# Optimization experiments

Measured on AMD Instinct MI355X. Metric: run time of the kernel, lower is better.

## Reference

```python
import jax, jax.numpy as jnp
import numpy as np

DIM = 16
BOND = 4
RANK = 512
N = 50000
E = 400000
F_IN = 16
EDGE_VARIABLE = 2


def setup_inputs() -> dict:
    key = jax.random.key(0)
    ks = iter(jax.random.split(key, 48))
    g = lambda shape, s=0.1: jax.random.normal(next(ks), shape, jnp.float32) * s
    inp = {
        "x": jax.random.normal(next(ks), (N, F_IN), jnp.float32),
        "node_type": jax.random.randint(next(ks), (N,), 0, 3),
        "edge_index": jax.random.randint(next(ks), (2, E), 0, N),
        "edge_attr": jax.random.uniform(next(ks), (E, BOND), dtype=jnp.float32),
        # lin0
        "W_lin0": g((F_IN, DIM)), "b_lin0": jnp.zeros((DIM,), jnp.float32),
        # NNConv: root weight + edge-conditioned weight MLP (4 -> 32 -> dim*dim)
        "W_root": g((DIM, DIM)), "b_conv": jnp.zeros((DIM,), jnp.float32),
        "W_e1": g((BOND, 32)), "b_e1": jnp.zeros((32,), jnp.float32),
        "W_e2": g((32, DIM * DIM)), "b_e2": jnp.zeros((DIM * DIM,), jnp.float32),
        # GRU (torch gate order r,z,n), weights stored torch-style [3*dim, dim]
        "W_ih": g((3 * DIM, DIM)), "b_ih": jnp.zeros((3 * DIM,), jnp.float32),
        "W_hh": g((3 * DIM, DIM)), "b_hh": jnp.zeros((3 * DIM,), jnp.float32),
        # projections
        "W_lin1": g((DIM, BOND)), "b_lin1": jnp.zeros((BOND,), jnp.float32),
        "W_up": g((BOND, DIM)), "b_up": jnp.zeros((DIM,), jnp.float32),
        "W_down": g((DIM, BOND)), "b_down": jnp.zeros((BOND,), jnp.float32),
        # FGNet low-rank factor modules (rank 512)
        "U_B": g((DIM, RANK)), "V_B": g((RANK, DIM)),
        "U_C": g((DIM, RANK)), "V_C": g((RANK, DIM)),
        "U_A": g((BOND, RANK)), "V_A": g((RANK, BOND)),
        # fusion weights
        "w_node": g((1, DIM)), "W_lin": g((DIM, DIM)), "b_lin": jnp.zeros((DIM,), jnp.float32),
        "w_edge": g((1, BOND)), "W_line": g((BOND, BOND)), "b_line": jnp.zeros((BOND,), jnp.float32),
    }
    return inp


def _forward(x, edge_attr, W_lin0, b_lin0, W_root, b_conv, W_e1, b_e1, W_e2, b_e2,
             W_ih, b_ih, W_hh, b_hh, W_lin1, b_lin1, W_up, b_up, W_down, b_down,
             U_B, V_B, U_C, V_C, U_A, V_A, w_node, W_lin, b_lin, w_edge, W_line, b_line,
             node_type, edge_index):
    src, dst = edge_index[0], edge_index[1]

    def nnconv(out):
        # per-edge weight matrices from edge features (edge-conditioned conv)
        he = jax.nn.relu(edge_attr @ W_e1 + b_e1)
        We = (he @ W_e2 + b_e2).reshape(E, DIM, DIM)          # [E, dim, dim]
        m = jnp.einsum('ed,edk->ek', out[src], We)             # gather-multiply
        agg = jax.ops.segment_sum(m, dst, num_segments=N)      # scatter-add
        deg = jax.ops.segment_sum(jnp.ones((E,), out.dtype), dst, num_segments=N)
        agg = agg / jnp.clip(deg, 1.0)[:, None]                # mean aggregation
        return out @ W_root + b_conv + agg

    def gru(inp, h):
        gi = inp @ W_ih.T + b_ih
        gh = h @ W_hh.T + b_hh
        i_r, i_z, i_n = jnp.split(gi, 3, axis=-1)
        h_r, h_z, h_n = jnp.split(gh, 3, axis=-1)
        r = jax.nn.sigmoid(i_r + h_r)
        z = jax.nn.sigmoid(i_z + h_z)
        n = jnp.tanh(i_n + r * h_n)
        return (1.0 - z) * n + z * h

    out = jax.nn.relu(x @ W_lin0 + b_lin0)                     # [N, dim]
    h = out
    for _ in range(3):
        m = jax.nn.relu(nnconv(out))
        h = gru(m, h)
        out = h

    out_edges = jax.nn.relu(out @ W_lin1 + b_lin1)             # [N, bond]

    # one outer message-passing round (k in range(1))
    ev_mask = (node_type == EDGE_VARIABLE)[:, None]
    out_edges_up = out_edges @ W_up + b_up                     # [N, dim]
    out_combine = jnp.where(ev_mask, out_edges_up, out)        # masked replace

    # factor-B message (low-rank FGNet) -> node-dim message + down-projected edge msg
    msg_B = jax.nn.relu((out_combine @ U_B) @ V_B)             # [N, dim]
    msg_to_edge_B = msg_B @ W_down + b_down                    # [N, bond]

    # factor-C message (low-rank FGNet)
    msg_C = jax.nn.relu((out_combine @ U_C) @ V_C)             # [N, dim]

    # factor-A / valence message on edge-type beliefs
    msg_to_edge_A = jax.nn.relu((out_edges @ U_A) @ V_A)       # [N, bond]

    all_msg = msg_B + msg_C                                    # sum over stacked msgs
    combine_edge_msg = msg_to_edge_A * msg_to_edge_B

    out = out + jax.nn.relu((w_node * all_msg) @ W_lin + b_lin)
    out_edges = out_edges + jax.nn.relu((w_edge * combine_edge_msg) @ W_line + b_line)

    return jax.nn.log_softmax(out_edges, axis=-1)              # [N, bond]


def reference(x, node_type, edge_index, edge_attr, W_lin0, b_lin0, W_root, b_conv,
              W_e1, b_e1, W_e2, b_e2, W_ih, b_ih, W_hh, b_hh, W_lin1, b_lin1,
              W_up, b_up, W_down, b_down, U_B, V_B, U_C, V_C, U_A, V_A,
              w_node, W_lin, b_lin, w_edge, W_line, b_line):
    return _forward(x, edge_attr, W_lin0, b_lin0, W_root, b_conv, W_e1, b_e1, W_e2, b_e2,
                    W_ih, b_ih, W_hh, b_hh, W_lin1, b_lin1, W_up, b_up, W_down, b_down,
                    U_B, V_B, U_C, V_C, U_A, V_A, w_node, W_lin, b_lin, w_edge, W_line, b_line,
                    node_type, edge_index)
```

## Files before the change

### kernel.cpp

```cpp
#include <hip/hip_runtime.h>
#include <hip/hip_bf16.h>
#include <math.h>

#define N_NODES 50000
#define N_EDGES 400000
#define DIM 16
#define BOND 4
#define NCHUNK 25000
#define EDGE_GRID 784
#define E_BLOCKS 1563
#define PRE_BASE (E_BLOCKS - 68)
#define SCAN_TILE 1024
#define SCAN_BLOCKS 49

typedef __attribute__((ext_vector_type(8))) short short8;
typedef __attribute__((ext_vector_type(4))) float f32x4;

__device__ __forceinline__ float bf16_to_f32(unsigned short v) {
  return __uint_as_float(((unsigned int)v) << 16);
}

__global__ __launch_bounds__(256) void setup_kernel(
    const float* __restrict__ x, const float* __restrict__ W_lin0,
    const float* __restrict__ b_lin0, const float* __restrict__ ea,
    const float* __restrict__ We1, const float* __restrict__ be1,
    const int* __restrict__ ei, const float* __restrict__ U_B,
    const float* __restrict__ V_B, const float* __restrict__ U_A,
    const float* __restrict__ V_A, float* __restrict__ out,
    unsigned int* __restrict__ he_buf, int* __restrict__ degI,
    int* __restrict__ rank, float* __restrict__ M_B, float* __restrict__ M_A) {
  __shared__ float sW0[256];
  __shared__ float sb0[16];
  __shared__ float sW1[128];
  __shared__ float sb1[32];
  int t = threadIdx.x;
  sW0[t] = W_lin0[t];
  if (t < 16) sb0[t] = b_lin0[t];
  if (t < 128) sW1[t] = We1[t];
  if (t < 32) sb1[t] = be1[t];
  __syncthreads();

  int gid = blockIdx.x * 256 + t;

  if (gid < N_NODES) {
    float xr[16];
#pragma unroll
    for (int d = 0; d < 16; ++d) xr[d] = x[gid * 16 + d];
#pragma unroll
    for (int k = 0; k < 16; ++k) {
      float acc = sb0[k];
#pragma unroll
      for (int d = 0; d < 16; ++d) acc += xr[d] * sW0[d * 16 + k];
      out[gid * 16 + k] = fmaxf(acc, 0.f);
    }
  }

  if (gid < N_EDGES) {
    float4 v = ((const float4*)ea)[gid];
    float h[32];
#pragma unroll
    for (int k = 0; k < 32; ++k) {
      float a = sb1[k] + v.x * sW1[k] + v.y * sW1[32 + k] + v.z * sW1[64 + k] +
                v.w * sW1[96 + k];
      h[k] = fmaxf(a, 0.f);
    }
    unsigned int u[16];
#pragma unroll
    for (int p = 0; p < 2; ++p)
#pragma unroll
      for (int tt = 0; tt < 8; ++tt) {
        float2 pr;
        pr.x = h[4 * tt + p];
        pr.y = h[4 * tt + 2 + p];
        __hip_bfloat162 b = __float22bfloat162_rn(pr);
        u[p * 8 + tt] = *(unsigned int*)&b;
      }
    uint4* dst = (uint4*)(he_buf + (size_t)gid * 16);
#pragma unroll
    for (int qq = 0; qq < 4; ++qq)
      dst[qq] =
          make_uint4(u[4 * qq], u[4 * qq + 1], u[4 * qq + 2], u[4 * qq + 3]);
    rank[gid] = atomicAdd(&degI[ei[N_EDGES + gid]], 1);
  }

  if (blockIdx.x >= PRE_BASE) {
    int w = (blockIdx.x - PRE_BASE) * 4 + (t >> 6);
    int lane = t & 63;
    float partial = 0.f;
    if (w < 256) {
      int i = w >> 4, j = w & 15;
#pragma unroll
      for (int r8 = 0; r8 < 8; ++r8) {
        int r = lane + 64 * r8;
        partial += U_B[i * 512 + r] * V_B[r * 16 + j];
      }
    } else if (w < 272) {
      int a = (w - 256) >> 2, b = (w - 256) & 3;
#pragma unroll
      for (int r8 = 0; r8 < 8; ++r8) {
        int r = lane + 64 * r8;
        partial += U_A[a * 512 + r] * V_A[r * 4 + b];
      }
    }
#pragma unroll
    for (int off = 32; off > 0; off >>= 1)
      partial += __shfl_down(partial, off);
    if (lane == 0) {
      if (w < 256) M_B[w] = partial;
      else if (w < 272) M_A[w - 256] = partial;
    }
  }
}

__global__ __launch_bounds__(256) void scan_kernel(
    const int* __restrict__ degI, int* ticket, int* st,
    int* __restrict__ row_off) {
  __shared__ int sdata[256];
  __shared__ int s_tile;
  __shared__ int s_base;
  int t = threadIdx.x;
  if (t == 0) s_tile = atomicAdd(ticket, 1);
  __syncthreads();
  int tile = s_tile;
  int n0 = tile * SCAN_TILE + t * 4;

  int d0 = (n0 + 0 < N_NODES) ? degI[n0 + 0] : 0;
  int d1 = (n0 + 1 < N_NODES) ? degI[n0 + 1] : 0;
  int d2 = (n0 + 2 < N_NODES) ? degI[n0 + 2] : 0;
  int d3 = (n0 + 3 < N_NODES) ? degI[n0 + 3] : 0;
  int tsum = d0 + d1 + d2 + d3;
  sdata[t] = tsum;
  __syncthreads();
  for (int off = 1; off < 256; off <<= 1) {
    int v = (t >= off) ? sdata[t - off] : 0;
    __syncthreads();
    sdata[t] += v;
    __syncthreads();
  }
  int excl = sdata[t] - tsum;
  int agg = sdata[255];

  if (t == 0) {
    if (tile == 0) {
      atomicExch(&st[0], (agg << 2) | 2);
      s_base = 0;
    } else {
      atomicExch(&st[tile], (agg << 2) | 1);
      int run = 0, idx = tile - 1;
      while (true) {
        int w = atomicAdd(&st[idx], 0);
        int stt = w & 3;
        if (stt == 2) { run += (w >> 2); break; }
        if (stt == 1) { run += (w >> 2); --idx; }
      }
      atomicExch(&st[tile], ((run + agg) << 2) | 2);
      s_base = run;
    }
  }
  __syncthreads();

  int pre = s_base + excl;
  if (n0 + 0 < N_NODES) row_off[n0 + 0] = pre;
  pre += d0;
  if (n0 + 1 < N_NODES) row_off[n0 + 1] = pre;
  pre += d1;
  if (n0 + 2 < N_NODES) row_off[n0 + 2] = pre;
  pre += d2;
  if (n0 + 3 < N_NODES) row_off[n0 + 3] = pre;
  if (tile == SCAN_BLOCKS - 1 && t == 0) row_off[N_NODES] = N_EDGES;
}

__global__ __launch_bounds__(256) void slot_kernel(
    const int* __restrict__ ei, const int* __restrict__ row_off,
    const int* __restrict__ rank, int* __restrict__ slot) {
  int e = blockIdx.x * 256 + threadIdx.x;
  if (e < N_EDGES) slot[e] = row_off[ei[N_EDGES + e]] + rank[e];
}

__global__ __launch_bounds__(256) void edge_msg_mfma_kernel(
    const int* __restrict__ ei, const unsigned int* __restrict__ he_buf,
    const float* __restrict__ We2, const float* __restrict__ be2,
    const float* __restrict__ out, const int* __restrict__ slot,
    unsigned short* __restrict__ m_bufh) {
  const int lane = threadIdx.x & 63;
  const int q = lane >> 4, n = lane & 15;
  const int p = q >> 1, dbase = (q & 1) * 8;

  short8 bfrag[17];
#pragma unroll
  for (int s = 0; s < 16; ++s) {
    int h = 2 * s + p;
    union { short8 v; __hip_bfloat162 b2[4]; } bf;
#pragma unroll
    for (int jj = 0; jj < 4; ++jj) {
      float2 w;
      w.x = We2[h * 256 + (dbase + 2 * jj) * 16 + n];
      w.y = We2[h * 256 + (dbase + 2 * jj + 1) * 16 + n];
      bf.b2[jj] = __float22bfloat162_rn(w);
    }
    bfrag[s] = bf.v;
  }
  {
    union { short8 v; __hip_bfloat162 b2[4]; } bf;
#pragma unroll
    for (int jj = 0; jj < 4; ++jj) {
      float2 w;
      if (q < 2) {
        w.x = be2[(dbase + 2 * jj) * 16 + n];
        w.y = be2[(dbase + 2 * jj + 1) * 16 + n];
      } else {
        w.x = 0.f; w.y = 0.f;
      }
      bf.b2[jj] = __float22bfloat162_rn(w);
    }
    bfrag[16] = bf.v;
  }

  int wave = blockIdx.x * 4 + (threadIdx.x >> 6);
  const int nw = EDGE_GRID * 4;
  for (int c = wave; c < NCHUNK; c += nw) {
    int e = c * 16 + n;
    int src = ei[e];
    const uint4* hp = (const uint4*)(he_buf + (size_t)e * 16 + p * 8);
    uint4 h0 = hp[0], h1 = hp[1];
    unsigned int heu[8] = {h0.x, h0.y, h0.z, h0.w, h1.x, h1.y, h1.z, h1.w};
    const float4* op = (const float4*)(out + src * 16 + dbase);
    float4 o0 = op[0], o1 = op[1];
    float o[8] = {o0.x, o0.y, o0.z, o0.w, o1.x, o1.y, o1.z, o1.w};

    f32x4 acc = {0.f, 0.f, 0.f, 0.f};
#pragma unroll
    for (int s = 0; s < 16; ++s) {
      unsigned int hw = heu[s >> 1];
      float he_s = __uint_as_float((s & 1) ? (hw & 0xffff0000u) : (hw << 16));
      union { short8 v; __hip_bfloat162 b2[4]; } af;
#pragma unroll
      for (int jj = 0; jj < 4; ++jj) {
        float2 pr;
        pr.x = he_s * o[2 * jj];
        pr.y = he_s * o[2 * jj + 1];
        af.b2[jj] = __float22bfloat162_rn(pr);
      }
      acc = __builtin_amdgcn_mfma_f32_16x16x32_bf16(af.v, bfrag[s], acc, 0, 0, 0);
    }
    {
      union { short8 v; __hip_bfloat162 b2[4]; } af;
#pragma unroll
      for (int jj = 0; jj < 4; ++jj) {
        float2 pr;
        if (q < 2) { pr.x = o[2 * jj]; pr.y = o[2 * jj + 1]; }
        else { pr.x = 0.f; pr.y = 0.f; }
        af.b2[jj] = __float22bfloat162_rn(pr);
      }
      acc = __builtin_amdgcn_mfma_f32_16x16x32_bf16(af.v, bfrag[16], acc, 0, 0, 0);
    }

    int4 sl4 = *(const int4*)(slot + c * 16 + q * 4);
    __hip_bfloat16 b0 = __float2bfloat16(acc[0]);
    __hip_bfloat16 b1 = __float2bfloat16(acc[1]);
    __hip_bfloat16 b2 = __float2bfloat16(acc[2]);
    __hip_bfloat16 b3 = __float2bfloat16(acc[3]);
    m_bufh[(size_t)sl4.x * 16 + n] = *(unsigned short*)&b0;
    m_bufh[(size_t)sl4.y * 16 + n] = *(unsigned short*)&b1;
    m_bufh[(size_t)sl4.z * 16 + n] = *(unsigned short*)&b2;
    m_bufh[(size_t)sl4.w * 16 + n] = *(unsigned short*)&b3;
  }
}

__global__ __launch_bounds__(256) void gather_gru_kernel(
    const int* __restrict__ row_off, const unsigned short* __restrict__ m_bufh,
    const float* __restrict__ Wroot, const float* __restrict__ bconv,
    const float* __restrict__ Wih, const float* __restrict__ bih,
    const float* __restrict__ Whh, const float* __restrict__ bhh,
    float* __restrict__ out, int do_final, const int* __restrict__ node_type,
    const float* __restrict__ Wlin1, const float* __restrict__ blin1,
    const float* __restrict__ Wup, const float* __restrict__ bup,
    const float* __restrict__ Wdown, const float* __restrict__ bdown,
    const float* __restrict__ M_B, const float* __restrict__ M_A,
    const float* __restrict__ wedge, const float* __restrict__ Wline,
    const float* __restrict__ bline, float* __restrict__ res) {
  __shared__ float sWr[256];
  __shared__ float sWihT[768];
  __shared__ float sWhhT[768];
  __shared__ float sb[112];
  int t = threadIdx.x;
  int kk = t >> 4, dd = t & 15;
  sWr[t] = Wroot[t];
#pragma unroll
  for (int g = 0; g < 3; ++g) {
    sWihT[g * 256 + dd * 16 + kk] = Wih[g * 256 + t];
    sWhhT[g * 256 + dd * 16 + kk] = Whh[g * 256 + t];
  }
  if (t < 16) sb[t] = bconv[t];
  else if (t < 64) sb[t] = bih[t - 16];
  else if (t < 112) sb[t] = bhh[t - 64];
  __syncthreads();

  int n = blockIdx.x * 16 + (t >> 4);
  int k = t & 15;
  int s0 = row_off[n], s1 = row_off[n + 1];

  float aggk = 0.f;
  for (int j = s0; j < s1; ++j) aggk += bf16_to_f32(m_bufh[(size_t)j * 16 + k]);
  float sc = 1.f / fmaxf((float)(s1 - s0), 1.f);

  float hk = out[n * 16 + k];

  float mk = sb[k] + aggk * sc;
#pragma unroll
  for (int d = 0; d < 16; ++d) mk += __shfl(hk, d, 16) * sWr[d * 16 + k];
  mk = fmaxf(mk, 0.f);

  float gir = sb[16 + k], giz = sb[32 + k], gin = sb[48 + k];
  float ghr = sb[64 + k], ghz = sb[80 + k], ghn = sb[96 + k];
#pragma unroll
  for (int d = 0; d < 16; ++d) {
    float md = __shfl(mk, d, 16);
    float hd = __shfl(hk, d, 16);
    gir += md * sWihT[d * 16 + k];
    giz += md * sWihT[256 + d * 16 + k];
    gin += md * sWihT[512 + d * 16 + k];
    ghr += hd * sWhhT[d * 16 + k];
    ghz += hd * sWhhT[256 + d * 16 + k];
    ghn += hd * sWhhT[512 + d * 16 + k];
  }
  float r = 1.f / (1.f + __expf(-(gir + ghr)));
  float z = 1.f / (1.f + __expf(-(giz + ghz)));
  float xn = gin + r * ghn;
  float ng = 1.f - 2.f / (__expf(2.f * xn) + 1.f);
  float hnew = (1.f - z) * ng + z * hk;

  if (!do_final) {
    out[n * 16 + k] = hnew;
    return;
  }

  float p0 = hnew * Wlin1[k * 4 + 0];
  float p1 = hnew * Wlin1[k * 4 + 1];
  float p2 = hnew * Wlin1[k * 4 + 2];
  float p3 = hnew * Wlin1[k * 4 + 3];
#pragma unroll
  for (int msk = 1; msk < 16; msk <<= 1) {
    p0 += __shfl_xor(p0, msk, 16);
    p1 += __shfl_xor(p1, msk, 16);
    p2 += __shfl_xor(p2, msk, 16);
    p3 += __shfl_xor(p3, msk, 16);
  }
  float oe0 = fmaxf(p0 + blin1[0], 0.f);
  float oe1 = fmaxf(p1 + blin1[1], 0.f);
  float oe2 = fmaxf(p2 + blin1[2], 0.f);
  float oe3 = fmaxf(p3 + blin1[3], 0.f);

  bool ev = (node_type[n] == 2);
  float ock = ev ? (bup[k] + oe0 * Wup[k] + oe1 * Wup[16 + k] +
                    oe2 * Wup[32 + k] + oe3 * Wup[48 + k])
                 : hnew;

  float msgBk = 0.f;
#pragma unroll
  for (int d = 0; d < 16; ++d) msgBk += __shfl(ock, d, 16) * M_B[d * 16 + k];
  msgBk = fmaxf(msgBk, 0.f);

  float q0 = msgBk * Wdown[k * 4 + 0];
  float q1 = msgBk * Wdown[k * 4 + 1];
  float q2 = msgBk * Wdown[k * 4 + 2];
  float q3 = msgBk * Wdown[k * 4 + 3];
#pragma unroll
  for (int msk = 1; msk < 16; msk <<= 1) {
    q0 += __shfl_xor(q0, msk, 16);
    q1 += __shfl_xor(q1, msk, 16);
    q2 += __shfl_xor(q2, msk, 16);
    q3 += __shfl_xor(q3, msk, 16);
  }
  float mtb0 = q0 + bdown[0], mtb1 = q1 + bdown[1];
  float mtb2 = q2 + bdown[2], mtb3 = q3 + bdown[3];

  float mta0 = fmaxf(oe0 * M_A[0] + oe1 * M_A[4] + oe2 * M_A[8] + oe3 * M_A[12], 0.f);
  float mta1 = fmaxf(oe0 * M_A[1] + oe1 * M_A[5] + oe2 * M_A[9] + oe3 * M_A[13], 0.f);
  float mta2 = fmaxf(oe0 * M_A[2] + oe1 * M_A[6] + oe2 * M_A[10] + oe3 * M_A[14], 0.f);
  float mta3 = fmaxf(oe0 * M_A[3] + oe1 * M_A[7] + oe2 * M_A[11] + oe3 * M_A[15], 0.f);

  float c0 = wedge[0] * (mta0 * mtb0);
  float c1 = wedge[1] * (mta1 * mtb1);
  float c2 = wedge[2] * (mta2 * mtb2);
  float c3 = wedge[3] * (mta3 * mtb3);

  float f0 = oe0 + fmaxf(bline[0] + c0 * Wline[0] + c1 * Wline[4] +
                         c2 * Wline[8] + c3 * Wline[12], 0.f);
  float f1 = oe1 + fmaxf(bline[1] + c0 * Wline[1] + c1 * Wline[5] +
                         c2 * Wline[9] + c3 * Wline[13], 0.f);
  float f2 = oe2 + fmaxf(bline[2] + c0 * Wline[2] + c1 * Wline[6] +
                         c2 * Wline[10] + c3 * Wline[14], 0.f);
  float f3 = oe3 + fmaxf(bline[3] + c0 * Wline[3] + c1 * Wline[7] +
                         c2 * Wline[11] + c3 * Wline[15], 0.f);

  float mx = fmaxf(fmaxf(f0, f1), fmaxf(f2, f3));
  float se = __expf(f0 - mx) + __expf(f1 - mx) + __expf(f2 - mx) +
             __expf(f3 - mx);
  float lse = mx + __logf(se);
  if (k < 4) {
    float v = (k == 0) ? f0 : (k == 1) ? f1 : (k == 2) ? f2 : f3;
    res[n * 4 + k] = v - lse;
  }
}

extern "C" void kernel_launch(void* const* d_in, const int* in_sizes, int n_in,
                              void* d_out, int out_size, void* d_ws,
                              size_t ws_size, hipStream_t stream) {
  const float* x       = (const float*)d_in[0];
  const int* node_type = (const int*)d_in[1];
  const int* ei        = (const int*)d_in[2];
  const float* ea      = (const float*)d_in[3];
  const float* W_lin0  = (const float*)d_in[4];
  const float* b_lin0  = (const float*)d_in[5];
  const float* W_root  = (const float*)d_in[6];
  const float* b_conv  = (const float*)d_in[7];
  const float* W_e1    = (const float*)d_in[8];
  const float* b_e1    = (const float*)d_in[9];
  const float* W_e2    = (const float*)d_in[10];
  const float* b_e2    = (const float*)d_in[11];
  const float* W_ih    = (const float*)d_in[12];
  const float* b_ih    = (const float*)d_in[13];
  const float* W_hh    = (const float*)d_in[14];
  const float* b_hh    = (const float*)d_in[15];
  const float* W_lin1  = (const float*)d_in[16];
  const float* b_lin1  = (const float*)d_in[17];
  const float* W_up    = (const float*)d_in[18];
  const float* b_up    = (const float*)d_in[19];
  const float* W_down  = (const float*)d_in[20];
  const float* b_down  = (const float*)d_in[21];
  const float* U_B     = (const float*)d_in[22];
  const float* V_B     = (const float*)d_in[23];
  const float* U_A     = (const float*)d_in[26];
  const float* V_A     = (const float*)d_in[27];
  const float* w_edge  = (const float*)d_in[31];
  const float* W_line  = (const float*)d_in[32];
  const float* b_line  = (const float*)d_in[33];

  float* ws    = (float*)d_ws;
  float* out   = ws;
  unsigned int* he_buf = (unsigned int*)(out + N_NODES * 16);
  unsigned short* m_bufh =
      (unsigned short*)(he_buf + (size_t)N_EDGES * 16);
  float* M_B   = (float*)(m_bufh + (size_t)N_EDGES * 16);
  float* M_A   = M_B + 256;
  int* degI    = (int*)(M_A + 16);
  int* ticket  = degI + N_NODES;
  int* st      = ticket + 1;
  int* row_off = st + 63;
  int* rank    = row_off + N_NODES + 1;
  int* slot    = rank + N_EDGES;

  hipMemsetAsync(degI, 0, (N_NODES + 64) * sizeof(int), stream);

  setup_kernel<<<E_BLOCKS, 256, 0, stream>>>(
      x, W_lin0, b_lin0, ea, W_e1, b_e1, ei, U_B, V_B, U_A, V_A, out, he_buf,
      degI, rank, M_B, M_A);
  scan_kernel<<<SCAN_BLOCKS, 256, 0, stream>>>(degI, ticket, st, row_off);
  slot_kernel<<<E_BLOCKS, 256, 0, stream>>>(ei, row_off, rank, slot);

  for (int it = 0; it < 3; ++it) {
    edge_msg_mfma_kernel<<<EDGE_GRID, 256, 0, stream>>>(ei, he_buf, W_e2, b_e2,
                                                        out, slot, m_bufh);
    gather_gru_kernel<<<N_NODES / 16, 256, 0, stream>>>(
        row_off, m_bufh, W_root, b_conv, W_ih, b_ih, W_hh, b_hh, out,
        (it == 2) ? 1 : 0, node_type, W_lin1, b_lin1, W_up, b_up, W_down,
        b_down, M_B, M_A, w_edge, W_line, b_line, (float*)d_out);
  }
}
```

Baseline: 330.1 us.

## Fuse scan, slot, and three message/GRU iterations into one persistent kernel

```diff
diff --git a/kernel.cpp b/kernel.cpp
--- a/kernel.cpp
+++ b/kernel.cpp
@@ -7,17 +7,43 @@
 #define DIM 16
 #define BOND 4
 #define NCHUNK 25000
-#define EDGE_GRID 784
 #define E_BLOCKS 1563
 #define PRE_BASE (E_BLOCKS - 68)
 #define SCAN_TILE 1024
 #define SCAN_BLOCKS 49
+#define FUSED_BLOCKS 768
+#define NGROUPS 3125
 
 typedef __attribute__((ext_vector_type(8))) short short8;
 typedef __attribute__((ext_vector_type(4))) float f32x4;
 
 __device__ __forceinline__ float bf16_to_f32(unsigned short v) {
   return __uint_as_float(((unsigned int)v) << 16);
+}
+
+__device__ __forceinline__ void grid_sync(int* bar_count, int* bar_gen) {
+  __syncthreads();
+  if (threadIdx.x == 0) {
+    __threadfence();
+    int g = __hip_atomic_load(bar_gen, __ATOMIC_RELAXED, __HIP_MEMORY_SCOPE_AGENT);
+    int old = __hip_atomic_fetch_add(bar_count, 1, __ATOMIC_ACQ_REL,
+                                     __HIP_MEMORY_SCOPE_AGENT);
+    if (old == FUSED_BLOCKS - 1) {
+      __hip_atomic_store(bar_count, 0, __ATOMIC_RELAXED,
+                         __HIP_MEMORY_SCOPE_AGENT);
+      __hip_atomic_fetch_add(bar_gen, 1, __ATOMIC_RELEASE,
+                             __HIP_MEMORY_SCOPE_AGENT);
+    } else {
+      long long t0 = clock64();
+      while (__hip_atomic_load(bar_gen, __ATOMIC_RELAXED,
+                               __HIP_MEMORY_SCOPE_AGENT) == g) {
+        __builtin_amdgcn_s_sleep(2);
+        if (clock64() - t0 > 100000000LL) break;
+      }
+    }
+    __threadfence();
+  }
+  __syncthreads();
 }
 
 __global__ __launch_bounds__(256) void setup_kernel(
@@ -112,77 +138,44 @@
   }
 }
 
-__global__ __launch_bounds__(256) void scan_kernel(
-    const int* __restrict__ degI, int* ticket, int* st,
-    int* __restrict__ row_off) {
-  __shared__ int sdata[256];
-  __shared__ int s_tile;
-  __shared__ int s_base;
-  int t = threadIdx.x;
-  if (t == 0) s_tile = atomicAdd(ticket, 1);
-  __syncthreads();
-  int tile = s_tile;
-  int n0 = tile * SCAN_TILE + t * 4;
-
-  int d0 = (n0 + 0 < N_NODES) ? degI[n0 + 0] : 0;
-  int d1 = (n0 + 1 < N_NODES) ? degI[n0 + 1] : 0;
-  int d2 = (n0 + 2 < N_NODES) ? degI[n0 + 2] : 0;
-  int d3 = (n0 + 3 < N_NODES) ? degI[n0 + 3] : 0;
-  int tsum = d0 + d1 + d2 + d3;
-  sdata[t] = tsum;
-  __syncthreads();
-  for (int off = 1; off < 256; off <<= 1) {
-    int v = (t >= off) ? sdata[t - off] : 0;
-    __syncthreads();
-    sdata[t] += v;
-    __syncthreads();
-  }
-  int excl = sdata[t] - tsum;
-  int agg = sdata[255];
-
-  if (t == 0) {
-    if (tile == 0) {
-      atomicExch(&st[0], (agg << 2) | 2);
-      s_base = 0;
-    } else {
-      atomicExch(&st[tile], (agg << 2) | 1);
-      int run = 0, idx = tile - 1;
-      while (true) {
-        int w = atomicAdd(&st[idx], 0);
-        int stt = w & 3;
-        if (stt == 2) { run += (w >> 2); break; }
-        if (stt == 1) { run += (w >> 2); --idx; }
-      }
-      atomicExch(&st[tile], ((run + agg) << 2) | 2);
-      s_base = run;
-    }
-  }
-  __syncthreads();
-
-  int pre = s_base + excl;
-  if (n0 + 0 < N_NODES) row_off[n0 + 0] = pre;
-  pre += d0;
-  if (n0 + 1 < N_NODES) row_off[n0 + 1] = pre;
-  pre += d1;
-  if (n0 + 2 < N_NODES) row_off[n0 + 2] = pre;
-  pre += d2;
-  if (n0 + 3 < N_NODES) row_off[n0 + 3] = pre;
-  if (tile == SCAN_BLOCKS - 1 && t == 0) row_off[N_NODES] = N_EDGES;
-}
-
-__global__ __launch_bounds__(256) void slot_kernel(
-    const int* __restrict__ ei, const int* __restrict__ row_off,
-    const int* __restrict__ rank, int* __restrict__ slot) {
-  int e = blockIdx.x * 256 + threadIdx.x;
-  if (e < N_EDGES) slot[e] = row_off[ei[N_EDGES + e]] + rank[e];
-}
-
-__global__ __launch_bounds__(256) void edge_msg_mfma_kernel(
+__global__ __launch_bounds__(256, 3) void fused_kernel(
     const int* __restrict__ ei, const unsigned int* __restrict__ he_buf,
     const float* __restrict__ We2, const float* __restrict__ be2,
-    const float* __restrict__ out, const int* __restrict__ slot,
-    unsigned short* __restrict__ m_bufh) {
-  const int lane = threadIdx.x & 63;
+    float* __restrict__ out, unsigned short* __restrict__ m_bufh,
+    const int* __restrict__ degI, int* __restrict__ row_off,
+    const int* __restrict__ rank, int* __restrict__ slot,
+    int* __restrict__ st, int* __restrict__ bar_count,
+    int* __restrict__ bar_gen,
+    const float* __restrict__ Wroot, const float* __restrict__ bconv,
+    const float* __restrict__ Wih, const float* __restrict__ bih,
+    const float* __restrict__ Whh, const float* __restrict__ bhh,
+    const int* __restrict__ node_type, const float* __restrict__ Wlin1,
+    const float* __restrict__ blin1, const float* __restrict__ Wup,
+    const float* __restrict__ bup, const float* __restrict__ Wdown,
+    const float* __restrict__ bdown, const float* __restrict__ M_B,
+    const float* __restrict__ M_A, const float* __restrict__ wedge,
+    const float* __restrict__ Wline, const float* __restrict__ bline,
+    float* __restrict__ res) {
+  __shared__ float sWr[256];
+  __shared__ float sWihT[768];
+  __shared__ float sWhhT[768];
+  __shared__ float sb[112];
+  __shared__ int sdata[256];
+  int t = threadIdx.x;
+  {
+    int kk = t >> 4, dd = t & 15;
+    sWr[t] = Wroot[t];
+#pragma unroll
+    for (int g = 0; g < 3; ++g) {
+      sWihT[g * 256 + dd * 16 + kk] = Wih[g * 256 + t];
+      sWhhT[g * 256 + dd * 16 + kk] = Whh[g * 256 + t];
+    }
+    if (t < 16) sb[t] = bconv[t];
+    else if (t < 64) sb[t] = bih[t - 16];
+    else if (t < 112) sb[t] = bhh[t - 64];
+  }
+
+  const int lane = t & 63;
   const int q = lane >> 4, n = lane & 15;
   const int p = q >> 1, dbase = (q & 1) * 8;
 
@@ -215,192 +208,232 @@
     }
     bfrag[16] = bf.v;
   }
-
-  int wave = blockIdx.x * 4 + (threadIdx.x >> 6);
-  const int nw = EDGE_GRID * 4;
-  for (int c = wave; c < NCHUNK; c += nw) {
-    int e = c * 16 + n;
-    int src = ei[e];
-    const uint4* hp = (const uint4*)(he_buf + (size_t)e * 16 + p * 8);
-    uint4 h0 = hp[0], h1 = hp[1];
-    unsigned int heu[8] = {h0.x, h0.y, h0.z, h0.w, h1.x, h1.y, h1.z, h1.w};
-    const float4* op = (const float4*)(out + src * 16 + dbase);
-    float4 o0 = op[0], o1 = op[1];
-    float o[8] = {o0.x, o0.y, o0.z, o0.w, o1.x, o1.y, o1.z, o1.w};
-
-    f32x4 acc = {0.f, 0.f, 0.f, 0.f};
-#pragma unroll
-    for (int s = 0; s < 16; ++s) {
-      unsigned int hw = heu[s >> 1];
-      float he_s = __uint_as_float((s & 1) ? (hw & 0xffff0000u) : (hw << 16));
-      union { short8 v; __hip_bfloat162 b2[4]; } af;
-#pragma unroll
-      for (int jj = 0; jj < 4; ++jj) {
-        float2 pr;
-        pr.x = he_s * o[2 * jj];
-        pr.y = he_s * o[2 * jj + 1];
-        af.b2[jj] = __float22bfloat162_rn(pr);
-      }
-      acc = __builtin_amdgcn_mfma_f32_16x16x32_bf16(af.v, bfrag[s], acc, 0, 0, 0);
-    }
-    {
-      union { short8 v; __hip_bfloat162 b2[4]; } af;
-#pragma unroll
-      for (int jj = 0; jj < 4; ++jj) {
-        float2 pr;
-        if (q < 2) { pr.x = o[2 * jj]; pr.y = o[2 * jj + 1]; }
-        else { pr.x = 0.f; pr.y = 0.f; }
-        af.b2[jj] = __float22bfloat162_rn(pr);
-      }
-      acc = __builtin_amdgcn_mfma_f32_16x16x32_bf16(af.v, bfrag[16], acc, 0, 0, 0);
-    }
-
-    int4 sl4 = *(const int4*)(slot + c * 16 + q * 4);
-    __hip_bfloat16 b0 = __float2bfloat16(acc[0]);
-    __hip_bfloat16 b1 = __float2bfloat16(acc[1]);
-    __hip_bfloat16 b2 = __float2bfloat16(acc[2]);
-    __hip_bfloat16 b3 = __float2bfloat16(acc[3]);
-    m_bufh[(size_t)sl4.x * 16 + n] = *(unsigned short*)&b0;
-    m_bufh[(size_t)sl4.y * 16 + n] = *(unsigned short*)&b1;
-    m_bufh[(size_t)sl4.z * 16 + n] = *(unsigned short*)&b2;
-    m_bufh[(size_t)sl4.w * 16 + n] = *(unsigned short*)&b3;
-  }
-}
-
-__global__ __launch_bounds__(256) void gather_gru_kernel(
-    const int* __restrict__ row_off, const unsigned short* __restrict__ m_bufh,
-    const float* __restrict__ Wroot, const float* __restrict__ bconv,
-    const float* __restrict__ Wih, const float* __restrict__ bih,
-    const float* __restrict__ Whh, const float* __restrict__ bhh,
-    float* __restrict__ out, int do_final, const int* __restrict__ node_type,
-    const float* __restrict__ Wlin1, const float* __restrict__ blin1,
-    const float* __restrict__ Wup, const float* __restrict__ bup,
-    const float* __restrict__ Wdown, const float* __restrict__ bdown,
-    const float* __restrict__ M_B, const float* __restrict__ M_A,
-    const float* __restrict__ wedge, const float* __restrict__ Wline,
-    const float* __restrict__ bline, float* __restrict__ res) {
-  __shared__ float sWr[256];
-  __shared__ float sWihT[768];
-  __shared__ float sWhhT[768];
-  __shared__ float sb[112];
-  int t = threadIdx.x;
-  int kk = t >> 4, dd = t & 15;
-  sWr[t] = Wroot[t];
-#pragma unroll
-  for (int g = 0; g < 3; ++g) {
-    sWihT[g * 256 + dd * 16 + kk] = Wih[g * 256 + t];
-    sWhhT[g * 256 + dd * 16 + kk] = Whh[g * 256 + t];
-  }
-  if (t < 16) sb[t] = bconv[t];
-  else if (t < 64) sb[t] = bih[t - 16];
-  else if (t < 112) sb[t] = bhh[t - 64];
   __syncthreads();
 
-  int n = blockIdx.x * 16 + (t >> 4);
-  int k = t & 15;
-  int s0 = row_off[n], s1 = row_off[n + 1];
-
-  float aggk = 0.f;
-  for (int j = s0; j < s1; ++j) aggk += bf16_to_f32(m_bufh[(size_t)j * 16 + k]);
-  float sc = 1.f / fmaxf((float)(s1 - s0), 1.f);
-
-  float hk = out[n * 16 + k];
-
-  float mk = sb[k] + aggk * sc;
-#pragma unroll
-  for (int d = 0; d < 16; ++d) mk += __shfl(hk, d, 16) * sWr[d * 16 + k];
-  mk = fmaxf(mk, 0.f);
-
-  float gir = sb[16 + k], giz = sb[32 + k], gin = sb[48 + k];
-  float ghr = sb[64 + k], ghz = sb[80 + k], ghn = sb[96 + k];
-#pragma unroll
-  for (int d = 0; d < 16; ++d) {
-    float md = __shfl(mk, d, 16);
-    float hd = __shfl(hk, d, 16);
-    gir += md * sWihT[d * 16 + k];
-    giz += md * sWihT[256 + d * 16 + k];
-    gin += md * sWihT[512 + d * 16 + k];
-    ghr += hd * sWhhT[d * 16 + k];
-    ghz += hd * sWhhT[256 + d * 16 + k];
-    ghn += hd * sWhhT[512 + d * 16 + k];
-  }
-  float r = 1.f / (1.f + __expf(-(gir + ghr)));
-  float z = 1.f / (1.f + __expf(-(giz + ghz)));
-  float xn = gin + r * ghn;
-  float ng = 1.f - 2.f / (__expf(2.f * xn) + 1.f);
-  float hnew = (1.f - z) * ng + z * hk;
-
-  if (!do_final) {
-    out[n * 16 + k] = hnew;
-    return;
-  }
-
-  float p0 = hnew * Wlin1[k * 4 + 0];
-  float p1 = hnew * Wlin1[k * 4 + 1];
-  float p2 = hnew * Wlin1[k * 4 + 2];
-  float p3 = hnew * Wlin1[k * 4 + 3];
-#pragma unroll
-  for (int msk = 1; msk < 16; msk <<= 1) {
-    p0 += __shfl_xor(p0, msk, 16);
-    p1 += __shfl_xor(p1, msk, 16);
-    p2 += __shfl_xor(p2, msk, 16);
-    p3 += __shfl_xor(p3, msk, 16);
-  }
-  float oe0 = fmaxf(p0 + blin1[0], 0.f);
-  float oe1 = fmaxf(p1 + blin1[1], 0.f);
-  float oe2 = fmaxf(p2 + blin1[2], 0.f);
-  float oe3 = fmaxf(p3 + blin1[3], 0.f);
-
-  bool ev = (node_type[n] == 2);
-  float ock = ev ? (bup[k] + oe0 * Wup[k] + oe1 * Wup[16 + k] +
-                    oe2 * Wup[32 + k] + oe3 * Wup[48 + k])
-                 : hnew;
-
-  float msgBk = 0.f;
-#pragma unroll
-  for (int d = 0; d < 16; ++d) msgBk += __shfl(ock, d, 16) * M_B[d * 16 + k];
-  msgBk = fmaxf(msgBk, 0.f);
-
-  float q0 = msgBk * Wdown[k * 4 + 0];
-  float q1 = msgBk * Wdown[k * 4 + 1];
-  float q2 = msgBk * Wdown[k * 4 + 2];
-  float q3 = msgBk * Wdown[k * 4 + 3];
-#pragma unroll
-  for (int msk = 1; msk < 16; msk <<= 1) {
-    q0 += __shfl_xor(q0, msk, 16);
-    q1 += __shfl_xor(q1, msk, 16);
-    q2 += __shfl_xor(q2, msk, 16);
-    q3 += __shfl_xor(q3, msk, 16);
-  }
-  float mtb0 = q0 + bdown[0], mtb1 = q1 + bdown[1];
-  float mtb2 = q2 + bdown[2], mtb3 = q3 + bdown[3];
-
-  float mta0 = fmaxf(oe0 * M_A[0] + oe1 * M_A[4] + oe2 * M_A[8] + oe3 * M_A[12], 0.f);
-  float mta1 = fmaxf(oe0 * M_A[1] + oe1 * M_A[5] + oe2 * M_A[9] + oe3 * M_A[13], 0.f);
-  float mta2 = fmaxf(oe0 * M_A[2] + oe1 * M_A[6] + oe2 * M_A[10] + oe3 * M_A[14], 0.f);
-  float mta3 = fmaxf(oe0 * M_A[3] + oe1 * M_A[7] + oe2 * M_A[11] + oe3 * M_A[15], 0.f);
-
-  float c0 = wedge[0] * (mta0 * mtb0);
-  float c1 = wedge[1] * (mta1 * mtb1);
-  float c2 = wedge[2] * (mta2 * mtb2);
-  float c3 = wedge[3] * (mta3 * mtb3);
-
-  float f0 = oe0 + fmaxf(bline[0] + c0 * Wline[0] + c1 * Wline[4] +
-                         c2 * Wline[8] + c3 * Wline[12], 0.f);
-  float f1 = oe1 + fmaxf(bline[1] + c0 * Wline[1] + c1 * Wline[5] +
-                         c2 * Wline[9] + c3 * Wline[13], 0.f);
-  float f2 = oe2 + fmaxf(bline[2] + c0 * Wline[2] + c1 * Wline[6] +
-                         c2 * Wline[10] + c3 * Wline[14], 0.f);
-  float f3 = oe3 + fmaxf(bline[3] + c0 * Wline[3] + c1 * Wline[7] +
-                         c2 * Wline[11] + c3 * Wline[15], 0.f);
-
-  float mx = fmaxf(fmaxf(f0, f1), fmaxf(f2, f3));
-  float se = __expf(f0 - mx) + __expf(f1 - mx) + __expf(f2 - mx) +
-             __expf(f3 - mx);
-  float lse = mx + __logf(se);
-  if (k < 4) {
-    float v = (k == 0) ? f0 : (k == 1) ? f1 : (k == 2) ? f2 : f3;
-    res[n * 4 + k] = v - lse;
+  if (blockIdx.x < SCAN_BLOCKS) {
+    int tile = blockIdx.x;
+    int n0 = tile * SCAN_TILE + t * 4;
+
+    int d0 = (n0 + 0 < N_NODES) ? degI[n0 + 0] : 0;
+    int d1 = (n0 + 1 < N_NODES) ? degI[n0 + 1] : 0;
+    int d2 = (n0 + 2 < N_NODES) ? degI[n0 + 2] : 0;
+    int d3 = (n0 + 3 < N_NODES) ? degI[n0 + 3] : 0;
+    int tsum = d0 + d1 + d2 + d3;
+    sdata[t] = tsum;
+    __syncthreads();
+    for (int off = 1; off < 256; off <<= 1) {
+      int v = (t >= off) ? sdata[t - off] : 0;
+      __syncthreads();
+      sdata[t] += v;
+      __syncthreads();
+    }
+    int excl = sdata[t] - tsum;
+    int agg = sdata[255];
+
+    __shared__ int s_base;
+    if (t == 0) {
+      if (tile == 0) {
+        atomicExch(&st[0], (agg << 2) | 2);
+        s_base = 0;
+      } else {
+        atomicExch(&st[tile], (agg << 2) | 1);
+        int run = 0, idx = tile - 1;
+        while (true) {
+          int w = atomicAdd(&st[idx], 0);
+          int stt = w & 3;
+          if (stt == 2) { run += (w >> 2); break; }
+          if (stt == 1) { run += (w >> 2); --idx; }
+        }
+        atomicExch(&st[tile], ((run + agg) << 2) | 2);
+        s_base = run;
+      }
+    }
+    __syncthreads();
+
+    int pre = s_base + excl;
+    if (n0 + 0 < N_NODES) row_off[n0 + 0] = pre;
+    pre += d0;
+    if (n0 + 1 < N_NODES) row_off[n0 + 1] = pre;
+    pre += d1;
+    if (n0 + 2 < N_NODES) row_off[n0 + 2] = pre;
+    pre += d2;
+    if (n0 + 3 < N_NODES) row_off[n0 + 3] = pre;
+    if (tile == SCAN_BLOCKS - 1 && t == 0) row_off[N_NODES] = N_EDGES;
+  }
+
+  grid_sync(bar_count, bar_gen);
+
+  for (int e = blockIdx.x * 256 + t; e < N_EDGES; e += FUSED_BLOCKS * 256)
+    slot[e] = row_off[ei[N_EDGES + e]] + rank[e];
+
+  grid_sync(bar_count, bar_gen);
+
+  const int wave = blockIdx.x * 4 + (t >> 6);
+  const int nw = FUSED_BLOCKS * 4;
+
+  for (int it = 0; it < 3; ++it) {
+    for (int c = wave; c < NCHUNK; c += nw) {
+      int e = c * 16 + n;
+      int src = ei[e];
+      const uint4* hp = (const uint4*)(he_buf + (size_t)e * 16 + p * 8);
+      uint4 h0 = hp[0], h1 = hp[1];
+      unsigned int heu[8] = {h0.x, h0.y, h0.z, h0.w, h1.x, h1.y, h1.z, h1.w};
+      const float4* op = (const float4*)(out + src * 16 + dbase);
+      float4 o0 = op[0], o1 = op[1];
+      float o[8] = {o0.x, o0.y, o0.z, o0.w, o1.x, o1.y, o1.z, o1.w};
+
+      f32x4 acc = {0.f, 0.f, 0.f, 0.f};
+#pragma unroll
+      for (int s = 0; s < 16; ++s) {
+        unsigned int hw = heu[s >> 1];
+        float he_s = __uint_as_float((s & 1) ? (hw & 0xffff0000u) : (hw << 16));
+        union { short8 v; __hip_bfloat162 b2[4]; } af;
+#pragma unroll
+        for (int jj = 0; jj < 4; ++jj) {
+          float2 pr;
+          pr.x = he_s * o[2 * jj];
+          pr.y = he_s * o[2 * jj + 1];
+          af.b2[jj] = __float22bfloat162_rn(pr);
+        }
+        acc = __builtin_amdgcn_mfma_f32_16x16x32_bf16(af.v, bfrag[s], acc, 0, 0, 0);
+      }
+      {
+        union { short8 v; __hip_bfloat162 b2[4]; } af;
+#pragma unroll
+        for (int jj = 0; jj < 4; ++jj) {
+          float2 pr;
+          if (q < 2) { pr.x = o[2 * jj]; pr.y = o[2 * jj + 1]; }
+          else { pr.x = 0.f; pr.y = 0.f; }
+          af.b2[jj] = __float22bfloat162_rn(pr);
+        }
+        acc = __builtin_amdgcn_mfma_f32_16x16x32_bf16(af.v, bfrag[16], acc, 0, 0, 0);
+      }
+
+      int4 sl4 = *(const int4*)(slot + c * 16 + q * 4);
+      __hip_bfloat16 b0 = __float2bfloat16(acc[0]);
+      __hip_bfloat16 b1 = __float2bfloat16(acc[1]);
+      __hip_bfloat16 b2 = __float2bfloat16(acc[2]);
+      __hip_bfloat16 b3 = __float2bfloat16(acc[3]);
+      m_bufh[(size_t)sl4.x * 16 + n] = *(unsigned short*)&b0;
+      m_bufh[(size_t)sl4.y * 16 + n] = *(unsigned short*)&b1;
+      m_bufh[(size_t)sl4.z * 16 + n] = *(unsigned short*)&b2;
+      m_bufh[(size_t)sl4.w * 16 + n] = *(unsigned short*)&b3;
+    }
+
+    grid_sync(bar_count, bar_gen);
+
+    int do_final = (it == 2);
+    for (int g = blockIdx.x; g < NGROUPS; g += FUSED_BLOCKS) {
+      int nn = g * 16 + (t >> 4);
+      int k = t & 15;
+      int s0 = row_off[nn], s1 = row_off[nn + 1];
+
+      float aggk = 0.f;
+      for (int j = s0; j < s1; ++j)
+        aggk += bf16_to_f32(m_bufh[(size_t)j * 16 + k]);
+      float sc = 1.f / fmaxf((float)(s1 - s0), 1.f);
+
+      float hk = out[nn * 16 + k];
+
+      float mk = sb[k] + aggk * sc;
+#pragma unroll
+      for (int d = 0; d < 16; ++d) mk += __shfl(hk, d, 16) * sWr[d * 16 + k];
+      mk = fmaxf(mk, 0.f);
+
+      float gir = sb[16 + k], giz = sb[32 + k], gin = sb[48 + k];
+      float ghr = sb[64 + k], ghz = sb[80 + k], ghn = sb[96 + k];
+#pragma unroll
+      for (int d = 0; d < 16; ++d) {
+        float md = __shfl(mk, d, 16);
+        float hd = __shfl(hk, d, 16);
+        gir += md * sWihT[d * 16 + k];
+        giz += md * sWihT[256 + d * 16 + k];
+        gin += md * sWihT[512 + d * 16 + k];
+        ghr += hd * sWhhT[d * 16 + k];
+        ghz += hd * sWhhT[256 + d * 16 + k];
+        ghn += hd * sWhhT[512 + d * 16 + k];
+      }
+      float r = 1.f / (1.f + __expf(-(gir + ghr)));
+      float z = 1.f / (1.f + __expf(-(giz + ghz)));
+      float xn = gin + r * ghn;
+      float ng = 1.f - 2.f / (__expf(2.f * xn) + 1.f);
+      float hnew = (1.f - z) * ng + z * hk;
+
+      if (!do_final) {
+        out[nn * 16 + k] = hnew;
+      } else {
+        float p0 = hnew * Wlin1[k * 4 + 0];
+        float p1 = hnew * Wlin1[k * 4 + 1];
+        float p2 = hnew * Wlin1[k * 4 + 2];
+        float p3 = hnew * Wlin1[k * 4 + 3];
+#pragma unroll
+        for (int msk = 1; msk < 16; msk <<= 1) {
+          p0 += __shfl_xor(p0, msk, 16);
+          p1 += __shfl_xor(p1, msk, 16);
+          p2 += __shfl_xor(p2, msk, 16);
+          p3 += __shfl_xor(p3, msk, 16);
+        }
+        float oe0 = fmaxf(p0 + blin1[0], 0.f);
+        float oe1 = fmaxf(p1 + blin1[1], 0.f);
+        float oe2 = fmaxf(p2 + blin1[2], 0.f);
+        float oe3 = fmaxf(p3 + blin1[3], 0.f);
+
+        bool ev = (node_type[nn] == 2);
+        float ock = ev ? (bup[k] + oe0 * Wup[k] + oe1 * Wup[16 + k] +
+                          oe2 * Wup[32 + k] + oe3 * Wup[48 + k])
+                       : hnew;
+
+        float msgBk = 0.f;
+#pragma unroll
+        for (int d = 0; d < 16; ++d)
+          msgBk += __shfl(ock, d, 16) * M_B[d * 16 + k];
+        msgBk = fmaxf(msgBk, 0.f);
+
+        float q0 = msgBk * Wdown[k * 4 + 0];
+        float q1 = msgBk * Wdown[k * 4 + 1];
+        float q2 = msgBk * Wdown[k * 4 + 2];
+        float q3 = msgBk * Wdown[k * 4 + 3];
+#pragma unroll
+        for (int msk = 1; msk < 16; msk <<= 1) {
+          q0 += __shfl_xor(q0, msk, 16);
+          q1 += __shfl_xor(q1, msk, 16);
+          q2 += __shfl_xor(q2, msk, 16);
+          q3 += __shfl_xor(q3, msk, 16);
+        }
+        float mtb0 = q0 + bdown[0], mtb1 = q1 + bdown[1];
+        float mtb2 = q2 + bdown[2], mtb3 = q3 + bdown[3];
+
+        float mta0 = fmaxf(oe0 * M_A[0] + oe1 * M_A[4] + oe2 * M_A[8] + oe3 * M_A[12], 0.f);
+        float mta1 = fmaxf(oe0 * M_A[1] + oe1 * M_A[5] + oe2 * M_A[9] + oe3 * M_A[13], 0.f);
+        float mta2 = fmaxf(oe0 * M_A[2] + oe1 * M_A[6] + oe2 * M_A[10] + oe3 * M_A[14], 0.f);
+        float mta3 = fmaxf(oe0 * M_A[3] + oe1 * M_A[7] + oe2 * M_A[11] + oe3 * M_A[15], 0.f);
+
+        float c0 = wedge[0] * (mta0 * mtb0);
+        float c1 = wedge[1] * (mta1 * mtb1);
+        float c2 = wedge[2] * (mta2 * mtb2);
+        float c3 = wedge[3] * (mta3 * mtb3);
+
+        float f0 = oe0 + fmaxf(bline[0] + c0 * Wline[0] + c1 * Wline[4] +
+                               c2 * Wline[8] + c3 * Wline[12], 0.f);
+        float f1 = oe1 + fmaxf(bline[1] + c0 * Wline[1] + c1 * Wline[5] +
+                               c2 * Wline[9] + c3 * Wline[13], 0.f);
+        float f2 = oe2 + fmaxf(bline[2] + c0 * Wline[2] + c1 * Wline[6] +
+                               c2 * Wline[10] + c3 * Wline[14], 0.f);
+        float f3 = oe3 + fmaxf(bline[3] + c0 * Wline[3] + c1 * Wline[7] +
+                               c2 * Wline[11] + c3 * Wline[15], 0.f);
+
+        float mx = fmaxf(fmaxf(f0, f1), fmaxf(f2, f3));
+        float se = __expf(f0 - mx) + __expf(f1 - mx) + __expf(f2 - mx) +
+                   __expf(f3 - mx);
+        float lse = mx + __logf(se);
+        if (k < 4) {
+          float v = (k == 0) ? f0 : (k == 1) ? f1 : (k == 2) ? f2 : f3;
+          res[nn * 4 + k] = v - lse;
+        }
+      }
+    }
+
+    if (it < 2) grid_sync(bar_count, bar_gen);
   }
 }
 
@@ -451,20 +484,18 @@
   int* rank    = row_off + N_NODES + 1;
   int* slot    = rank + N_EDGES;
 
+  int* bar_count = ticket;
+  int* bar_gen   = st + 62;
+
   hipMemsetAsync(degI, 0, (N_NODES + 64) * sizeof(int), stream);
 
   setup_kernel<<<E_BLOCKS, 256, 0, stream>>>(
       x, W_lin0, b_lin0, ea, W_e1, b_e1, ei, U_B, V_B, U_A, V_A, out, he_buf,
       degI, rank, M_B, M_A);
-  scan_kernel<<<SCAN_BLOCKS, 256, 0, stream>>>(degI, ticket, st, row_off);
-  slot_kernel<<<E_BLOCKS, 256, 0, stream>>>(ei, row_off, rank, slot);
-
-  for (int it = 0; it < 3; ++it) {
-    edge_msg_mfma_kernel<<<EDGE_GRID, 256, 0, stream>>>(ei, he_buf, W_e2, b_e2,
-                                                        out, slot, m_bufh);
-    gather_gru_kernel<<<N_NODES / 16, 256, 0, stream>>>(
-        row_off, m_bufh, W_root, b_conv, W_ih, b_ih, W_hh, b_hh, out,
-        (it == 2) ? 1 : 0, node_type, W_lin1, b_lin1, W_up, b_up, W_down,
-        b_down, M_B, M_A, w_edge, W_line, b_line, (float*)d_out);
-  }
+
+  fused_kernel<<<FUSED_BLOCKS, 256, 0, stream>>>(
+      ei, he_buf, W_e2, b_e2, out, m_bufh, degI, row_off, rank, slot, st,
+      bar_count, bar_gen, W_root, b_conv, W_ih, b_ih, W_hh, b_hh, node_type,
+      W_lin1, b_lin1, W_up, b_up, W_down, b_down, M_B, M_A, w_edge, W_line,
+      b_line, (float*)d_out);
 }
```

After: 722.8 us. 2.19x slower.

## Recompute edge hidden layer in edge kernel and fold slot computation inline

Applied to the files above, without the earlier changes.

```diff
diff --git a/kernel.cpp b/kernel.cpp
--- a/kernel.cpp
+++ b/kernel.cpp
@@ -22,22 +22,16 @@
 
 __global__ __launch_bounds__(256) void setup_kernel(
     const float* __restrict__ x, const float* __restrict__ W_lin0,
-    const float* __restrict__ b_lin0, const float* __restrict__ ea,
-    const float* __restrict__ We1, const float* __restrict__ be1,
-    const int* __restrict__ ei, const float* __restrict__ U_B,
-    const float* __restrict__ V_B, const float* __restrict__ U_A,
-    const float* __restrict__ V_A, float* __restrict__ out,
-    unsigned int* __restrict__ he_buf, int* __restrict__ degI,
-    int* __restrict__ rank, float* __restrict__ M_B, float* __restrict__ M_A) {
+    const float* __restrict__ b_lin0, const int* __restrict__ ei,
+    const float* __restrict__ U_B, const float* __restrict__ V_B,
+    const float* __restrict__ U_A, const float* __restrict__ V_A,
+    float* __restrict__ out, int* __restrict__ degI, int* __restrict__ rank,
+    float* __restrict__ M_B, float* __restrict__ M_A) {
   __shared__ float sW0[256];
   __shared__ float sb0[16];
-  __shared__ float sW1[128];
-  __shared__ float sb1[32];
   int t = threadIdx.x;
   sW0[t] = W_lin0[t];
   if (t < 16) sb0[t] = b_lin0[t];
-  if (t < 128) sW1[t] = We1[t];
-  if (t < 32) sb1[t] = be1[t];
   __syncthreads();
 
   int gid = blockIdx.x * 256 + t;
@@ -56,30 +50,6 @@
   }
 
   if (gid < N_EDGES) {
-    float4 v = ((const float4*)ea)[gid];
-    float h[32];
-#pragma unroll
-    for (int k = 0; k < 32; ++k) {
-      float a = sb1[k] + v.x * sW1[k] + v.y * sW1[32 + k] + v.z * sW1[64 + k] +
-                v.w * sW1[96 + k];
-      h[k] = fmaxf(a, 0.f);
-    }
-    unsigned int u[16];
-#pragma unroll
-    for (int p = 0; p < 2; ++p)
-#pragma unroll
-      for (int tt = 0; tt < 8; ++tt) {
-        float2 pr;
-        pr.x = h[4 * tt + p];
-        pr.y = h[4 * tt + 2 + p];
-        __hip_bfloat162 b = __float22bfloat162_rn(pr);
-        u[p * 8 + tt] = *(unsigned int*)&b;
-      }
-    uint4* dst = (uint4*)(he_buf + (size_t)gid * 16);
-#pragma unroll
-    for (int qq = 0; qq < 4; ++qq)
-      dst[qq] =
-          make_uint4(u[4 * qq], u[4 * qq + 1], u[4 * qq + 2], u[4 * qq + 3]);
     rank[gid] = atomicAdd(&degI[ei[N_EDGES + gid]], 1);
   }
 
@@ -170,19 +140,19 @@
   if (tile == SCAN_BLOCKS - 1 && t == 0) row_off[N_NODES] = N_EDGES;
 }
 
-__global__ __launch_bounds__(256) void slot_kernel(
-    const int* __restrict__ ei, const int* __restrict__ row_off,
-    const int* __restrict__ rank, int* __restrict__ slot) {
-  int e = blockIdx.x * 256 + threadIdx.x;
-  if (e < N_EDGES) slot[e] = row_off[ei[N_EDGES + e]] + rank[e];
-}
-
 __global__ __launch_bounds__(256) void edge_msg_mfma_kernel(
-    const int* __restrict__ ei, const unsigned int* __restrict__ he_buf,
+    const int* __restrict__ ei, const float* __restrict__ ea,
+    const float* __restrict__ We1, const float* __restrict__ be1,
     const float* __restrict__ We2, const float* __restrict__ be2,
-    const float* __restrict__ out, const int* __restrict__ slot,
-    unsigned short* __restrict__ m_bufh) {
-  const int lane = threadIdx.x & 63;
+    const float* __restrict__ out, const int* __restrict__ row_off,
+    const int* __restrict__ rank, unsigned short* __restrict__ m_bufh) {
+  __shared__ float sW1T[128];
+  __shared__ float sbe1[32];
+  int t = threadIdx.x;
+  if (t < 128) sW1T[t] = We1[(t & 3) * 32 + 2 * ((t >> 2) & 15) + (t >> 6)];
+  if (t < 32) sbe1[t] = be1[2 * (t & 15) + (t >> 4)];
+
+  const int lane = t & 63;
   const int q = lane >> 4, n = lane & 15;
   const int p = q >> 1, dbase = (q & 1) * 8;
 
@@ -215,15 +185,21 @@
     }
     bfrag[16] = bf.v;
   }
-
-  int wave = blockIdx.x * 4 + (threadIdx.x >> 6);
+  __syncthreads();
+
+  int wave = blockIdx.x * 4 + (t >> 6);
   const int nw = EDGE_GRID * 4;
   for (int c = wave; c < NCHUNK; c += nw) {
-    int e = c * 16 + n;
+    int base = c * 16;
+    int e = base + n;
+    int4 dst4 = *(const int4*)(ei + N_EDGES + base + q * 4);
+    int4 rk4 = *(const int4*)(rank + base + q * 4);
     int src = ei[e];
-    const uint4* hp = (const uint4*)(he_buf + (size_t)e * 16 + p * 8);
-    uint4 h0 = hp[0], h1 = hp[1];
-    unsigned int heu[8] = {h0.x, h0.y, h0.z, h0.w, h1.x, h1.y, h1.z, h1.w};
+    float4 av = ((const float4*)ea)[e];
+    int slx = row_off[dst4.x] + rk4.x;
+    int sly = row_off[dst4.y] + rk4.y;
+    int slz = row_off[dst4.z] + rk4.z;
+    int slw = row_off[dst4.w] + rk4.w;
     const float4* op = (const float4*)(out + src * 16 + dbase);
     float4 o0 = op[0], o1 = op[1];
     float o[8] = {o0.x, o0.y, o0.z, o0.w, o1.x, o1.y, o1.z, o1.w};
@@ -231,8 +207,10 @@
     f32x4 acc = {0.f, 0.f, 0.f, 0.f};
 #pragma unroll
     for (int s = 0; s < 16; ++s) {
-      unsigned int hw = heu[s >> 1];
-      float he_s = __uint_as_float((s & 1) ? (hw & 0xffff0000u) : (hw << 16));
+      float4 wj = *(const float4*)&sW1T[(p * 16 + s) * 4];
+      float he_s = fmaxf(sbe1[p * 16 + s] + av.x * wj.x + av.y * wj.y +
+                             av.z * wj.z + av.w * wj.w,
+                         0.f);
       union { short8 v; __hip_bfloat162 b2[4]; } af;
 #pragma unroll
       for (int jj = 0; jj < 4; ++jj) {
@@ -255,15 +233,14 @@
       acc = __builtin_amdgcn_mfma_f32_16x16x32_bf16(af.v, bfrag[16], acc, 0, 0, 0);
     }
 
-    int4 sl4 = *(const int4*)(slot + c * 16 + q * 4);
     __hip_bfloat16 b0 = __float2bfloat16(acc[0]);
     __hip_bfloat16 b1 = __float2bfloat16(acc[1]);
     __hip_bfloat16 b2 = __float2bfloat16(acc[2]);
     __hip_bfloat16 b3 = __float2bfloat16(acc[3]);
-    m_bufh[(size_t)sl4.x * 16 + n] = *(unsigned short*)&b0;
-    m_bufh[(size_t)sl4.y * 16 + n] = *(unsigned short*)&b1;
-    m_bufh[(size_t)sl4.z * 16 + n] = *(unsigned short*)&b2;
-    m_bufh[(size_t)sl4.w * 16 + n] = *(unsigned short*)&b3;
+    m_bufh[(size_t)slx * 16 + n] = *(unsigned short*)&b0;
+    m_bufh[(size_t)sly * 16 + n] = *(unsigned short*)&b1;
+    m_bufh[(size_t)slz * 16 + n] = *(unsigned short*)&b2;
+    m_bufh[(size_t)slw * 16 + n] = *(unsigned short*)&b3;
   }
 }
 
@@ -439,9 +416,7 @@
 
   float* ws    = (float*)d_ws;
   float* out   = ws;
-  unsigned int* he_buf = (unsigned int*)(out + N_NODES * 16);
-  unsigned short* m_bufh =
-      (unsigned short*)(he_buf + (size_t)N_EDGES * 16);
+  unsigned short* m_bufh = (unsigned short*)(out + N_NODES * 16);
   float* M_B   = (float*)(m_bufh + (size_t)N_EDGES * 16);
   float* M_A   = M_B + 256;
   int* degI    = (int*)(M_A + 16);
@@ -449,19 +424,17 @@
   int* st      = ticket + 1;
   int* row_off = st + 63;
   int* rank    = row_off + N_NODES + 1;
-  int* slot    = rank + N_EDGES;
 
   hipMemsetAsync(degI, 0, (N_NODES + 64) * sizeof(int), stream);
 
-  setup_kernel<<<E_BLOCKS, 256, 0, stream>>>(
-      x, W_lin0, b_lin0, ea, W_e1, b_e1, ei, U_B, V_B, U_A, V_A, out, he_buf,
-      degI, rank, M_B, M_A);
+  setup_kernel<<<E_BLOCKS, 256, 0, stream>>>(x, W_lin0, b_lin0, ei, U_B, V_B,
+                                             U_A, V_A, out, degI, rank, M_B,
+                                             M_A);
   scan_kernel<<<SCAN_BLOCKS, 256, 0, stream>>>(degI, ticket, st, row_off);
-  slot_kernel<<<E_BLOCKS, 256, 0, stream>>>(ei, row_off, rank, slot);
 
   for (int it = 0; it < 3; ++it) {
-    edge_msg_mfma_kernel<<<EDGE_GRID, 256, 0, stream>>>(ei, he_buf, W_e2, b_e2,
-                                                        out, slot, m_bufh);
+    edge_msg_mfma_kernel<<<EDGE_GRID, 256, 0, stream>>>(
+        ei, ea, W_e1, b_e1, W_e2, b_e2, out, row_off, rank, m_bufh);
     gather_gru_kernel<<<N_NODES / 16, 256, 0, stream>>>(
         row_off, m_bufh, W_root, b_conv, W_ih, b_ih, W_hh, b_hh, out,
         (it == 2) ? 1 : 0, node_type, W_lin1, b_lin1, W_up, b_up, W_down,
```

Measured after the change: 360.2 us. 1.09x slower.
